# Performance work log

Measured on AMD Instinct MI355X. Metric: run time of the kernel, lower is better.

## Reference

```python
import jax, jax.numpy as jnp
import numpy as np

DIM = 384
H = 6
D = DIM // H
MLP = 4 * DIM
SCALE = D ** -0.5
LN_EPS = 1e-5


def _ln(x, w, b):
    m = jnp.mean(x, axis=-1, keepdims=True)
    v = jnp.mean((x - m) ** 2, axis=-1, keepdims=True)
    return (x - m) * jax.lax.rsqrt(v + LN_EPS) * w + b


def setup_inputs() -> dict:
    key = jax.random.key(0)
    ks = jax.random.split(key, 8)
    B, N = 8, 1024
    x = jax.random.normal(ks[0], (B, N, DIM), dtype=jnp.float32)
    # torch nn.Linear weights are [out, in]
    qkv_w = jax.random.normal(ks[1], (3 * DIM, DIM), dtype=jnp.float32) * (DIM ** -0.5)
    proj_w = jax.random.normal(ks[2], (DIM, DIM), dtype=jnp.float32) * (DIM ** -0.5)
    proj_b = jnp.zeros((DIM,), jnp.float32)
    # L2Q params, 'quadratic' init
    alpha = jnp.full((H, 1, 1), 0.125, jnp.float32)
    beta = jnp.full((H, 1, 1), 0.5, jnp.float32)
    gamma = jnp.zeros((H, 1, 1), jnp.float32)
    ln1_w = jnp.ones((DIM,), jnp.float32)
    ln1_b = jnp.zeros((DIM,), jnp.float32)
    ln2_w = jnp.ones((DIM,), jnp.float32)
    ln2_b = jnp.zeros((DIM,), jnp.float32)
    w1 = jax.random.normal(ks[3], (MLP, DIM), dtype=jnp.float32) * (DIM ** -0.5)
    b1 = jnp.zeros((MLP,), jnp.float32)
    w2 = jax.random.normal(ks[4], (DIM, MLP), dtype=jnp.float32) * (MLP ** -0.5)
    b2 = jnp.zeros((DIM,), jnp.float32)
    return {"x": x, "qkv_w": qkv_w, "proj_w": proj_w, "proj_b": proj_b,
            "alpha": alpha, "beta": beta, "gamma": gamma,
            "ln1_w": ln1_w, "ln1_b": ln1_b, "ln2_w": ln2_w, "ln2_b": ln2_b,
            "w1": w1, "b1": b1, "w2": w2, "b2": b2}


def reference(x, qkv_w, proj_w, proj_b, alpha, beta, gamma,
              ln1_w, ln1_b, ln2_w, ln2_b, w1, b1, w2, b2):
    B, N, C = x.shape
    # --- L2Q attention on LN(x) ---
    h = _ln(x, ln1_w, ln1_b)
    qkv = (h @ qkv_w.T).reshape(B, N, 3, H, D)
    q = qkv[:, :, 0].transpose(0, 2, 1, 3)  # [B,H,N,D]
    k = qkv[:, :, 1].transpose(0, 2, 1, 3)
    v = qkv[:, :, 2].transpose(0, 2, 1, 3)
    logits = jnp.einsum('bhnd,bhmd->bhnm', q, k) * SCALE
    attn = jax.nn.relu(alpha * logits ** 2 + beta * logits + gamma)
    attn = attn / (jnp.sum(attn, axis=-1, keepdims=True) + 1e-6)
    out = jnp.einsum('bhnm,bhmd->bhnd', attn, v)
    out = out.transpose(0, 2, 1, 3).reshape(B, N, C)
    x = x + out @ proj_w.T + proj_b
    # --- MLP on LN(x), exact GELU (torch default) ---
    h2 = _ln(x, ln2_w, ln2_b)
    m = jax.nn.gelu(h2 @ w1.T + b1, approximate=False)
    x = x + m @ w2.T + b2
    return x
```

## Files before the change

### kernel.cpp

```cpp
#include <hip/hip_runtime.h>
#include <hip/hip_bf16.h>
#include <math.h>

#define DIMC 384
#define NH 6
#define HD 64
#define MLPD 1536
#define BS 8
#define SEQ 1024
#define T_TOK (BS*SEQ)
#define TC ((size_t)T_TOK*DIMC)
#define QK_SCALE 0.125f

typedef __bf16 bf16;
typedef bf16 bf16x4 __attribute__((ext_vector_type(4)));
typedef bf16 bf16x8 __attribute__((ext_vector_type(8)));
typedef float floatx4 __attribute__((ext_vector_type(4)));

__device__ __forceinline__ void async_cp16(const void* gsrc, void* ldst) {
    __builtin_amdgcn_global_load_lds(
        (const __attribute__((address_space(1))) unsigned int*)gsrc,
        (__attribute__((address_space(3))) unsigned int*)ldst,
        16, 0, 0);
}

__global__ __launch_bounds__(256)
void cvt_all(const float* __restrict__ s0, const float* __restrict__ s1,
             const float* __restrict__ s2, const float* __restrict__ s3,
             bf16* __restrict__ dst) {
    int i = blockIdx.x * 256 + threadIdx.x;
    const int n0 = 110592, n1 = 36864, n2 = 147456;
    const float4* src; int j;
    if (i < n0)           { src = (const float4*)s0; j = i; }
    else if (i < n0+n1)   { src = (const float4*)s1; j = i - n0; }
    else if (i < n0+n1+n2){ src = (const float4*)s2; j = i - n0 - n1; }
    else                  { src = (const float4*)s3; j = i - n0 - n1 - n2; }
    float4 v = src[j];
    bf16x4 o; o[0] = (bf16)v.x; o[1] = (bf16)v.y; o[2] = (bf16)v.z; o[3] = (bf16)v.w;
    ((bf16x4*)dst)[i] = o;
}

__global__ __launch_bounds__(256)
void ln_kernel(const float* __restrict__ x, const float* __restrict__ w,
               const float* __restrict__ b, bf16* __restrict__ out) {
    int row = blockIdx.x * 4 + (threadIdx.x >> 6);
    int t = threadIdx.x & 63;
    const float* xr = x + (size_t)row * DIMC;
    float vals[6];
    float s = 0.f;
    #pragma unroll
    for (int i = 0; i < 6; i++) { vals[i] = xr[t + i*64]; s += vals[i]; }
    #pragma unroll
    for (int m = 32; m; m >>= 1) s += __shfl_xor(s, m);
    float mean = s * (1.0f / DIMC);
    float sq = 0.f;
    #pragma unroll
    for (int i = 0; i < 6; i++) { float d = vals[i] - mean; sq += d * d; }
    #pragma unroll
    for (int m = 32; m; m >>= 1) sq += __shfl_xor(sq, m);
    float rstd = rsqrtf(sq * (1.0f / DIMC) + 1e-5f);
    bf16* orow = out + (size_t)row * DIMC;
    #pragma unroll
    for (int i = 0; i < 6; i++) {
        int c = t + i*64;
        orow[c] = (bf16)((vals[i] - mean) * rstd * w[c] + b[c]);
    }
}

__global__ __launch_bounds__(256)
void ln2_fused(const float* __restrict__ x, const bf16* __restrict__ p0,
               const bf16* __restrict__ p1, const float* __restrict__ pb,
               const float* __restrict__ w, const float* __restrict__ b,
               float* __restrict__ x1, bf16* __restrict__ h) {
    int row = blockIdx.x * 4 + (threadIdx.x >> 6);
    int t = threadIdx.x & 63;
    size_t base = (size_t)row * DIMC;
    float vals[6];
    float s = 0.f;
    #pragma unroll
    for (int i = 0; i < 6; i++) {
        int c = t + i*64;
        float v = x[base + c] + (float)p0[base + c] + (float)p1[base + c] + pb[c];
        vals[i] = v; s += v;
    }
    #pragma unroll
    for (int m = 32; m; m >>= 1) s += __shfl_xor(s, m);
    float mean = s * (1.0f / DIMC);
    float sq = 0.f;
    #pragma unroll
    for (int i = 0; i < 6; i++) { float d = vals[i] - mean; sq += d * d; }
    #pragma unroll
    for (int m = 32; m; m >>= 1) sq += __shfl_xor(sq, m);
    float rstd = rsqrtf(sq * (1.0f / DIMC) + 1e-5f);
    #pragma unroll
    for (int i = 0; i < 6; i++) {
        int c = t + i*64;
        x1[base + c] = vals[i];
        h[base + c] = (bf16)((vals[i] - mean) * rstd * w[c] + b[c]);
    }
}

__global__ __launch_bounds__(256)
void reduce4(float* __restrict__ xo, const bf16* __restrict__ p0, const bf16* __restrict__ p1,
             const bf16* __restrict__ p2, const bf16* __restrict__ p3,
             const float* __restrict__ b2) {
    int i = blockIdx.x * 256 + threadIdx.x;
    float4 v = ((const float4*)xo)[i];
    int c = (i % 96) * 4;
    float4 bb = *(const float4*)(b2 + c);
    bf16x4 a0 = ((const bf16x4*)p0)[i], a1 = ((const bf16x4*)p1)[i];
    bf16x4 a2 = ((const bf16x4*)p2)[i], a3 = ((const bf16x4*)p3)[i];
    v.x += bb.x + (float)a0[0] + (float)a1[0] + (float)a2[0] + (float)a3[0];
    v.y += bb.y + (float)a0[1] + (float)a1[1] + (float)a2[1] + (float)a3[1];
    v.z += bb.z + (float)a0[2] + (float)a1[2] + (float)a2[2] + (float)a3[2];
    v.w += bb.w + (float)a0[3] + (float)a1[3] + (float)a2[3] + (float)a3[3];
    ((float4*)xo)[i] = v;
}

enum { EPI_NONE = 0, EPI_QKV = 1, EPI_GELU = 3 };

template<int EPI, int K, int KS, typename OutT>
__global__ __launch_bounds__(256)
void gemm_bt(const bf16* __restrict__ A, const bf16* __restrict__ W,
             const float* __restrict__ bias, OutT* out, int M, int N) {
    __shared__ __align__(16) bf16 Ash[128*32];
    __shared__ __align__(16) bf16 Bsh[128*32];
    constexpr int KB = K / KS;
    int tid = threadIdx.x;
    int lane = tid & 63, w = tid >> 6;
    int quad = lane >> 4, l16 = lane & 15;
    int rbase = blockIdx.y * 128 + (w >> 1) * 64;
    int cbase = blockIdx.x * 128 + (w & 1) * 64;
    int kbase = blockIdx.z * KB;
    int c1 = w * 64 + lane;
    int c2 = c1 + 256;
    const bf16* Ag1 = A + (size_t)(blockIdx.y*128 + (c1 >> 2)) * K + kbase + (c1 & 3) * 8;
    const bf16* Ag2 = A + (size_t)(blockIdx.y*128 + (c2 >> 2)) * K + kbase + (c2 & 3) * 8;
    const bf16* Wg1 = W + (size_t)(blockIdx.x*128 + (c1 >> 2)) * K + kbase + (c1 & 3) * 8;
    const bf16* Wg2 = W + (size_t)(blockIdx.x*128 + (c2 >> 2)) * K + kbase + (c2 & 3) * 8;
    bf16* As1 = Ash + c1 * 8;  bf16* As2 = Ash + c2 * 8;
    bf16* Bs1 = Bsh + c1 * 8;  bf16* Bs2 = Bsh + c2 * 8;

    int arow = (w >> 1) * 64;
    int brow = (w & 1) * 64;
    floatx4 acc[4][4] = {};
    #pragma unroll
    for (int kk = 0; kk < KB / 32; kk++) {
        __syncthreads();
        async_cp16(Ag1 + kk*32, As1);
        async_cp16(Ag2 + kk*32, As2);
        async_cp16(Wg1 + kk*32, Bs1);
        async_cp16(Wg2 + kk*32, Bs2);
        __syncthreads();
        bf16x8 a[4], bfr[4];
        #pragma unroll
        for (int tm = 0; tm < 4; tm++)
            a[tm] = *(const bf16x8*)&Ash[(arow + tm*16 + l16) * 32 + quad*8];
        #pragma unroll
        for (int tn = 0; tn < 4; tn++)
            bfr[tn] = *(const bf16x8*)&Bsh[(brow + tn*16 + l16) * 32 + quad*8];
        #pragma unroll
        for (int tm = 0; tm < 4; tm++)
            #pragma unroll
            for (int tn = 0; tn < 4; tn++)
                acc[tm][tn] = __builtin_amdgcn_mfma_f32_16x16x32_bf16(a[tm], bfr[tn], acc[tm][tn], 0, 0, 0);
    }

    #pragma unroll
    for (int tm = 0; tm < 4; tm++)
        #pragma unroll
        for (int tn = 0; tn < 4; tn++) {
            if constexpr (EPI == EPI_QKV) {
                int colb = cbase + tn*16 + l16;
                int which = colb / 384;
                int rowb = rbase + tm*16 + quad*4;
                int bb = rowb >> 10;
                if (which == 2) {
                    int rem = colb - 768;
                    int hh = rem >> 6, d = rem & 63;
                    int n = rowb & 1023;
                    bf16x4 pk;
                    #pragma unroll
                    for (int r = 0; r < 4; r++) pk[r] = (bf16)acc[tm][tn][r];
                    *(bf16x4*)((bf16*)out + 2*TC + (((size_t)(bb*NH + hh) * HD + d) << 10) + n) = pk;
                } else {
                    int rem = colb - which*384;
                    int hh = rem >> 6, d = rem & 63;
                    #pragma unroll
                    for (int r = 0; r < 4; r++) {
                        int n = (rowb & 1023) + r;
                        ((bf16*)out)[(size_t)which*TC + (((size_t)(bb*NH + hh) * SEQ + n) << 6) + d]
                            = (bf16)acc[tm][tn][r];
                    }
                }
            } else if constexpr (EPI == EPI_NONE) {
                OutT* ob = out + (size_t)blockIdx.z * M * N;
                #pragma unroll
                for (int r = 0; r < 4; r++) {
                    int row = rbase + tm*16 + quad*4 + r;
                    int col = cbase + tn*16 + l16;
                    ob[(size_t)row * N + col] = (OutT)acc[tm][tn][r];
                }
            } else {
                #pragma unroll
                for (int r = 0; r < 4; r++) {
                    int row = rbase + tm*16 + quad*4 + r;
                    int col = cbase + tn*16 + l16;
                    float v = acc[tm][tn][r] + bias[col];
                    v = 0.5f * v * (1.0f + erff(v * 0.70710678118f));
                    out[(size_t)row * N + col] = (OutT)v;
                }
            }
        }
}

__global__ __launch_bounds__(256)
void attn_kernel(const bf16* __restrict__ q, const bf16* __restrict__ k,
                 const bf16* __restrict__ vt, const float* __restrict__ alpha,
                 const float* __restrict__ beta, const float* __restrict__ gamma,
                 bf16* __restrict__ attn_out) {
    __shared__ __align__(16) char smem[52992];
    bf16  (*Psh)[72] = (bf16(*)[72])smem;
    float (*Ored)[68] = (float(*)[68])smem;
    float* rsred = (float*)(smem + 52224);

    int L = blockIdx.x;
    int xcd = L & 7, slot = L >> 3;
    int qt = slot & 15;
    int bh = xcd + ((slot >> 4) << 3);
    int bb = bh / NH, h = bh % NH;
    int q0 = qt * 64;
    int tid = threadIdx.x;
    int w = tid >> 6, lane = tid & 63, quad = lane >> 4, l16 = lane & 15;
    float av = alpha[h] * (QK_SCALE * QK_SCALE), bv = beta[h] * QK_SCALE, gv = gamma[h];
    const bf16* qb  = q  + (size_t)bh * SEQ * HD;
    const bf16* kb  = k  + (size_t)bh * SEQ * HD;
    const bf16* vtb = vt + (size_t)bh * HD * SEQ;

    bf16x8 qa[4][2];
    #pragma unroll
    for (int tm = 0; tm < 4; tm++)
        #pragma unroll
        for (int ks = 0; ks < 2; ks++)
            qa[tm][ks] = *(const bf16x8*)(qb + (size_t)(q0 + tm*16 + l16) * HD + ks*32 + quad*8);

    bf16x8 vone;
    #pragma unroll
    for (int j = 0; j < 8; j++) vone[j] = (bf16)1.0f;

    floatx4 o[4][4] = {};
    floatx4 rsacc[4] = {};
    int prow = w * 64;
    int rd_sw = ((l16 >> 2) & 3) << 3;

    for (int kt = w*4; kt < w*4 + 4; kt++) {
        int kb0 = kt * 64;
        bf16x8 kf[2][4];
        #pragma unroll
        for (int ks = 0; ks < 2; ks++)
            #pragma unroll
            for (int tn = 0; tn < 4; tn++)
                kf[ks][tn] = *(const bf16x8*)(kb + (size_t)(kb0 + tn*16 + l16) * HD + ks*32 + quad*8);
        #pragma unroll
        for (int tm = 0; tm < 4; tm++) {
            floatx4 s[4] = {};
            #pragma unroll
            for (int ks = 0; ks < 2; ks++)
                #pragma unroll
                for (int tn = 0; tn < 4; tn++)
                    s[tn] = __builtin_amdgcn_mfma_f32_16x16x32_bf16(qa[tm][ks], kf[ks][tn], s[tn], 0, 0, 0);
            #pragma unroll
            for (int tn = 0; tn < 4; tn++)
                #pragma unroll
                for (int r = 0; r < 4; r++) {
                    float xx = s[tn][r];
                    float p = fmaxf((av*xx + bv)*xx + gv, 0.f);
                    int row = tm*16 + quad*4 + r;
                    int col = (tn*16 + l16) ^ (quad << 3);
                    Psh[prow + row][col] = (bf16)p;
                }
        }
        #pragma unroll
        for (int ks = 0; ks < 2; ks++) {
            bf16x8 vf[4], pf[4];
            #pragma unroll
            for (int tn = 0; tn < 4; tn++)
                vf[tn] = *(const bf16x8*)(vtb + (size_t)(tn*16 + l16) * SEQ + kb0 + ks*32 + quad*8);
            #pragma unroll
            for (int tm = 0; tm < 4; tm++)
                pf[tm] = *(const bf16x8*)&Psh[prow + tm*16 + l16][(ks*32 + quad*8) ^ rd_sw];
            #pragma unroll
            for (int tm = 0; tm < 4; tm++)
                rsacc[tm] = __builtin_amdgcn_mfma_f32_16x16x32_bf16(pf[tm], vone, rsacc[tm], 0, 0, 0);
            #pragma unroll
            for (int tm = 0; tm < 4; tm++)
                #pragma unroll
                for (int tn = 0; tn < 4; tn++)
                    o[tm][tn] = __builtin_amdgcn_mfma_f32_16x16x32_bf16(pf[tm], vf[tn], o[tm][tn], 0, 0, 0);
        }
    }

    __syncthreads();
    if (w) {
        #pragma unroll
        for (int tm = 0; tm < 4; tm++) {
            #pragma unroll
            for (int tn = 0; tn < 4; tn++)
                #pragma unroll
                for (int r = 0; r < 4; r++)
                    Ored[(w-1)*64 + tm*16 + quad*4 + r][tn*16 + l16] = o[tm][tn][r];
            if (l16 == 0)
                #pragma unroll
                for (int r = 0; r < 4; r++)
                    rsred[(w-1)*64 + tm*16 + quad*4 + r] = rsacc[tm][r];
        }
    }
    __syncthreads();
    if (w == 0) {
        #pragma unroll
        for (int j = 0; j < 3; j++)
            #pragma unroll
            for (int tm = 0; tm < 4; tm++) {
                #pragma unroll
                for (int tn = 0; tn < 4; tn++)
                    #pragma unroll
                    for (int r = 0; r < 4; r++)
                        o[tm][tn][r] += Ored[j*64 + tm*16 + quad*4 + r][tn*16 + l16];
                #pragma unroll
                for (int r = 0; r < 4; r++)
                    rsacc[tm][r] += rsred[j*64 + tm*16 + quad*4 + r];
            }
        #pragma unroll
        for (int tm = 0; tm < 4; tm++)
            #pragma unroll
            for (int tn = 0; tn < 4; tn++)
                #pragma unroll
                for (int r = 0; r < 4; r++) {
                    int n = q0 + tm*16 + quad*4 + r;
                    attn_out[((size_t)(bb*SEQ + n)) * DIMC + h*HD + tn*16 + l16] =
                        (bf16)(o[tm][tn][r] / (rsacc[tm][r] + 1e-6f));
                }
    }
}

extern "C" void kernel_launch(void* const* d_in, const int* in_sizes, int n_in,
                              void* d_out, int out_size, void* d_ws, size_t ws_size,
                              hipStream_t stream) {
    const float* x      = (const float*)d_in[0];
    const float* qkv_w  = (const float*)d_in[1];
    const float* proj_w = (const float*)d_in[2];
    const float* proj_b = (const float*)d_in[3];
    const float* alpha  = (const float*)d_in[4];
    const float* beta   = (const float*)d_in[5];
    const float* gamma  = (const float*)d_in[6];
    const float* ln1_w  = (const float*)d_in[7];
    const float* ln1_b  = (const float*)d_in[8];
    const float* ln2_w  = (const float*)d_in[9];
    const float* ln2_b  = (const float*)d_in[10];
    const float* w1     = (const float*)d_in[11];
    const float* b1     = (const float*)d_in[12];
    const float* w2     = (const float*)d_in[13];
    const float* b2     = (const float*)d_in[14];
    float* out = (float*)d_out;

    char* base = (char*)d_ws;
    bf16* wq_bf = (bf16*)base;
    bf16* wp_bf = wq_bf + 442368;
    bf16* w1_bf = wq_bf + 589824;
    bf16* w2_bf = wq_bf + 1179648;
    bf16* h      = (bf16*)(base + 3538944);
    bf16* qkv    = (bf16*)(base + 9830400);
    bf16* attn_o = (bf16*)(base + 28704768);
    bf16* m      = qkv;
    bf16* Pp     = (bf16*)(base + 34996224);
    bf16* Pm     = (bf16*)(base + 34996224);

    cvt_all<<<1728, 256, 0, stream>>>(qkv_w, proj_w, w1, w2, wq_bf);
    ln_kernel<<<T_TOK/4, 256, 0, stream>>>(x, ln1_w, ln1_b, h);
    gemm_bt<EPI_QKV, 384, 1, bf16><<<dim3(9, 64, 1), 256, 0, stream>>>(
        h, wq_bf, nullptr, qkv, T_TOK, 1152);
    attn_kernel<<<768, 256, 0, stream>>>(
        qkv, qkv + TC, qkv + 2*TC, alpha, beta, gamma, attn_o);
    gemm_bt<EPI_NONE, 384, 2, bf16><<<dim3(3, 64, 2), 256, 0, stream>>>(
        attn_o, wp_bf, nullptr, Pp, T_TOK, DIMC);
    ln2_fused<<<T_TOK/4, 256, 0, stream>>>(x, Pp, Pp + TC, proj_b, ln2_w, ln2_b, out, h);
    gemm_bt<EPI_GELU, 384, 1, bf16><<<dim3(12, 64, 1), 256, 0, stream>>>(
        h, w1_bf, b1, m, T_TOK, MLPD);
    gemm_bt<EPI_NONE, 1536, 4, bf16><<<dim3(3, 64, 4), 256, 0, stream>>>(
        m, w2_bf, nullptr, Pm, T_TOK, DIMC);
    reduce4<<<TC/4/256, 256, 0, stream>>>(out, Pm, Pm + TC, Pm + 2*TC, Pm + 3*TC, b2);
}
```

Measured before the change: 244.0 us.

## Prefetch K tiles in attention and use tree reduction across waves

The attention kernel now fully unrolls the per-wave key-tile loop and issues the next tile's K loads ahead of the current tile's compute. V fragments are loaded before the score computation so their latency overlaps the QK MFMAs. The final cross-wave reduction becomes a two-level tree, with row sums stored in an extra column and the output rows split between two waves, which shrinks shared memory and spreads the epilogue. This adds register pressure from the kn and vf buffers and one more barrier.

```diff
diff --git a/kernel.cpp b/kernel.cpp
--- a/kernel.cpp
+++ b/kernel.cpp
@@ -219,10 +219,10 @@
                  const bf16* __restrict__ vt, const float* __restrict__ alpha,
                  const float* __restrict__ beta, const float* __restrict__ gamma,
                  bf16* __restrict__ attn_out) {
-    __shared__ __align__(16) char smem[52992];
+    __shared__ __align__(16) char smem[36864];
     bf16  (*Psh)[72] = (bf16(*)[72])smem;
-    float (*Ored)[68] = (float(*)[68])smem;
-    float* rsred = (float*)(smem + 52224);
+    float (*RedA)[68] = (float(*)[68])smem;
+    float (*RedB)[68] = RedA + 64;
 
     int L = blockIdx.x;
     int xcd = L & 7, slot = L >> 3;
@@ -252,15 +252,31 @@
     floatx4 rsacc[4] = {};
     int prow = w * 64;
     int rd_sw = ((l16 >> 2) & 3) << 3;
-
-    for (int kt = w*4; kt < w*4 + 4; kt++) {
-        int kb0 = kt * 64;
-        bf16x8 kf[2][4];
+    int kt_base = w * 4;
+
+    bf16x8 kf[2][4], kn[2][4], vf[2][4];
+    #pragma unroll
+    for (int ks = 0; ks < 2; ks++)
+        #pragma unroll
+        for (int tn = 0; tn < 4; tn++)
+            kf[ks][tn] = *(const bf16x8*)(kb + (size_t)(kt_base*64 + tn*16 + l16) * HD + ks*32 + quad*8);
+
+    #pragma unroll
+    for (int t = 0; t < 4; t++) {
+        int kb0 = (kt_base + t) * 64;
+        if (t < 3) {
+            int nb0 = kb0 + 64;
+            #pragma unroll
+            for (int ks = 0; ks < 2; ks++)
+                #pragma unroll
+                for (int tn = 0; tn < 4; tn++)
+                    kn[ks][tn] = *(const bf16x8*)(kb + (size_t)(nb0 + tn*16 + l16) * HD + ks*32 + quad*8);
+        }
         #pragma unroll
         for (int ks = 0; ks < 2; ks++)
             #pragma unroll
             for (int tn = 0; tn < 4; tn++)
-                kf[ks][tn] = *(const bf16x8*)(kb + (size_t)(kb0 + tn*16 + l16) * HD + ks*32 + quad*8);
+                vf[ks][tn] = *(const bf16x8*)(vtb + (size_t)(tn*16 + l16) * SEQ + kb0 + ks*32 + quad*8);
         #pragma unroll
         for (int tm = 0; tm < 4; tm++) {
             floatx4 s[4] = {};
@@ -282,10 +298,7 @@
         }
         #pragma unroll
         for (int ks = 0; ks < 2; ks++) {
-            bf16x8 vf[4], pf[4];
-            #pragma unroll
-            for (int tn = 0; tn < 4; tn++)
-                vf[tn] = *(const bf16x8*)(vtb + (size_t)(tn*16 + l16) * SEQ + kb0 + ks*32 + quad*8);
+            bf16x8 pf[4];
             #pragma unroll
             for (int tm = 0; tm < 4; tm++)
                 pf[tm] = *(const bf16x8*)&Psh[prow + tm*16 + l16][(ks*32 + quad*8) ^ rd_sw];
@@ -296,50 +309,109 @@
             for (int tm = 0; tm < 4; tm++)
                 #pragma unroll
                 for (int tn = 0; tn < 4; tn++)
-                    o[tm][tn] = __builtin_amdgcn_mfma_f32_16x16x32_bf16(pf[tm], vf[tn], o[tm][tn], 0, 0, 0);
+                    o[tm][tn] = __builtin_amdgcn_mfma_f32_16x16x32_bf16(pf[tm], vf[ks][tn], o[tm][tn], 0, 0, 0);
+        }
+        if (t < 3) {
+            #pragma unroll
+            for (int ks = 0; ks < 2; ks++)
+                #pragma unroll
+                for (int tn = 0; tn < 4; tn++)
+                    kf[ks][tn] = kn[ks][tn];
         }
     }
 
     __syncthreads();
-    if (w) {
+    if (w & 1) {
+        float (*R)[68] = (w == 1) ? RedA : RedB;
         #pragma unroll
         for (int tm = 0; tm < 4; tm++) {
             #pragma unroll
             for (int tn = 0; tn < 4; tn++)
                 #pragma unroll
                 for (int r = 0; r < 4; r++)
-                    Ored[(w-1)*64 + tm*16 + quad*4 + r][tn*16 + l16] = o[tm][tn][r];
+                    R[tm*16 + quad*4 + r][tn*16 + l16] = o[tm][tn][r];
             if (l16 == 0)
                 #pragma unroll
                 for (int r = 0; r < 4; r++)
-                    rsred[(w-1)*64 + tm*16 + quad*4 + r] = rsacc[tm][r];
+                    R[tm*16 + quad*4 + r][64] = rsacc[tm][r];
+        }
+    }
+    __syncthreads();
+    if (!(w & 1)) {
+        float (*R)[68] = (w == 0) ? RedA : RedB;
+        #pragma unroll
+        for (int tm = 0; tm < 4; tm++) {
+            #pragma unroll
+            for (int tn = 0; tn < 4; tn++)
+                #pragma unroll
+                for (int r = 0; r < 4; r++)
+                    o[tm][tn][r] += R[tm*16 + quad*4 + r][tn*16 + l16];
+            #pragma unroll
+            for (int r = 0; r < 4; r++)
+                rsacc[tm][r] += R[tm*16 + quad*4 + r][64];
+        }
+    }
+    __syncthreads();
+    if (w == 2) {
+        #pragma unroll
+        for (int tm = 0; tm < 2; tm++) {
+            #pragma unroll
+            for (int tn = 0; tn < 4; tn++)
+                #pragma unroll
+                for (int r = 0; r < 4; r++)
+                    RedA[tm*16 + quad*4 + r][tn*16 + l16] = o[tm][tn][r];
+            if (l16 == 0)
+                #pragma unroll
+                for (int r = 0; r < 4; r++)
+                    RedA[tm*16 + quad*4 + r][64] = rsacc[tm][r];
+        }
+    } else if (w == 0) {
+        #pragma unroll
+        for (int tm = 2; tm < 4; tm++) {
+            #pragma unroll
+            for (int tn = 0; tn < 4; tn++)
+                #pragma unroll
+                for (int r = 0; r < 4; r++)
+                    RedA[tm*16 + quad*4 + r][tn*16 + l16] = o[tm][tn][r];
+            if (l16 == 0)
+                #pragma unroll
+                for (int r = 0; r < 4; r++)
+                    RedA[tm*16 + quad*4 + r][64] = rsacc[tm][r];
         }
     }
     __syncthreads();
     if (w == 0) {
         #pragma unroll
-        for (int j = 0; j < 3; j++)
-            #pragma unroll
-            for (int tm = 0; tm < 4; tm++) {
-                #pragma unroll
-                for (int tn = 0; tn < 4; tn++)
-                    #pragma unroll
-                    for (int r = 0; r < 4; r++)
-                        o[tm][tn][r] += Ored[j*64 + tm*16 + quad*4 + r][tn*16 + l16];
-                #pragma unroll
-                for (int r = 0; r < 4; r++)
-                    rsacc[tm][r] += rsred[j*64 + tm*16 + quad*4 + r];
-            }
-        #pragma unroll
-        for (int tm = 0; tm < 4; tm++)
+        for (int tm = 0; tm < 2; tm++) {
+            #pragma unroll
+            for (int r = 0; r < 4; r++)
+                rsacc[tm][r] += RedA[tm*16 + quad*4 + r][64];
             #pragma unroll
             for (int tn = 0; tn < 4; tn++)
                 #pragma unroll
                 for (int r = 0; r < 4; r++) {
+                    float ov = o[tm][tn][r] + RedA[tm*16 + quad*4 + r][tn*16 + l16];
                     int n = q0 + tm*16 + quad*4 + r;
                     attn_out[((size_t)(bb*SEQ + n)) * DIMC + h*HD + tn*16 + l16] =
-                        (bf16)(o[tm][tn][r] / (rsacc[tm][r] + 1e-6f));
-                }
+                        (bf16)(ov / (rsacc[tm][r] + 1e-6f));
+                }
+        }
+    } else if (w == 2) {
+        #pragma unroll
+        for (int tm = 2; tm < 4; tm++) {
+            #pragma unroll
+            for (int r = 0; r < 4; r++)
+                rsacc[tm][r] += RedA[tm*16 + quad*4 + r][64];
+            #pragma unroll
+            for (int tn = 0; tn < 4; tn++)
+                #pragma unroll
+                for (int r = 0; r < 4; r++) {
+                    float ov = o[tm][tn][r] + RedA[tm*16 + quad*4 + r][tn*16 + l16];
+                    int n = q0 + tm*16 + quad*4 + r;
+                    attn_out[((size_t)(bb*SEQ + n)) * DIMC + h*HD + tn*16 + l16] =
+                        (bf16)(ov / (rsacc[tm][r] + 1e-6f));
+                }
+        }
     }
 }
 
```

Result: faster. 233.2 us (-4.4%).

## Restructure attention: split PV across head-dim per wave with shared P tiles

Applied to the files above, without the earlier changes.

Changes the attention kernel so that each wave computes scores for its own 64-key slice of a 256-key chunk into a shared P tile. All four waves then split the PV product along the head dimension, 16 output columns each, rather than each wave owning a quarter of the keys and reducing full 64x64 outputs through LDS at the end. Row sums are taken directly from the fp32 probabilities with shuffles instead of an extra MFMA against a ones vector. It also requests 2 blocks per SM through launch_bounds. The cost is two __syncthreads per chunk, and it drops the LDS swizzle, which may add bank conflicts.

```diff
diff --git a/kernel.cpp b/kernel.cpp
--- a/kernel.cpp
+++ b/kernel.cpp
@@ -214,15 +214,14 @@
         }
 }
 
-__global__ __launch_bounds__(256)
+__global__ __launch_bounds__(256, 2)
 void attn_kernel(const bf16* __restrict__ q, const bf16* __restrict__ k,
                  const bf16* __restrict__ vt, const float* __restrict__ alpha,
                  const float* __restrict__ beta, const float* __restrict__ gamma,
                  bf16* __restrict__ attn_out) {
-    __shared__ __align__(16) char smem[52992];
-    bf16  (*Psh)[72] = (bf16(*)[72])smem;
-    float (*Ored)[68] = (float(*)[68])smem;
-    float* rsred = (float*)(smem + 52224);
+    __shared__ __align__(16) bf16 Psh[64][264];
+    __shared__ float rsW[4][64];
+    __shared__ float rs_final[64];
 
     int L = blockIdx.x;
     int xcd = L & 7, slot = L >> 3;
@@ -237,110 +236,90 @@
     const bf16* kb  = k  + (size_t)bh * SEQ * HD;
     const bf16* vtb = vt + (size_t)bh * HD * SEQ;
 
-    bf16x8 qa[4][2];
-    #pragma unroll
-    for (int tm = 0; tm < 4; tm++)
-        #pragma unroll
-        for (int ks = 0; ks < 2; ks++)
-            qa[tm][ks] = *(const bf16x8*)(qb + (size_t)(q0 + tm*16 + l16) * HD + ks*32 + quad*8);
-
-    bf16x8 vone;
-    #pragma unroll
-    for (int j = 0; j < 8; j++) vone[j] = (bf16)1.0f;
-
-    floatx4 o[4][4] = {};
-    floatx4 rsacc[4] = {};
-    int prow = w * 64;
-    int rd_sw = ((l16 >> 2) & 3) << 3;
-
-    for (int kt = w*4; kt < w*4 + 4; kt++) {
-        int kb0 = kt * 64;
-        bf16x8 kf[2][4];
-        #pragma unroll
-        for (int ks = 0; ks < 2; ks++)
-            #pragma unroll
-            for (int tn = 0; tn < 4; tn++)
-                kf[ks][tn] = *(const bf16x8*)(kb + (size_t)(kb0 + tn*16 + l16) * HD + ks*32 + quad*8);
-        #pragma unroll
-        for (int tm = 0; tm < 4; tm++) {
+    floatx4 o[4] = {};
+    float rsp[4] = {0.f, 0.f, 0.f, 0.f};
+
+    bf16x8 kf[2][4];
+    #pragma unroll
+    for (int ks = 0; ks < 2; ks++)
+        #pragma unroll
+        for (int ksub = 0; ksub < 4; ksub++)
+            kf[ks][ksub] = *(const bf16x8*)(kb + (size_t)(w*64 + ksub*16 + l16) * HD + ks*32 + quad*8);
+
+    for (int c = 0; c < 4; c++) {
+        #pragma unroll
+        for (int qsub = 0; qsub < 4; qsub++) {
+            bf16x8 qa0 = *(const bf16x8*)(qb + (size_t)(q0 + qsub*16 + l16) * HD + quad*8);
+            bf16x8 qa1 = *(const bf16x8*)(qb + (size_t)(q0 + qsub*16 + l16) * HD + 32 + quad*8);
             floatx4 s[4] = {};
+            #pragma unroll
+            for (int ksub = 0; ksub < 4; ksub++)
+                s[ksub] = __builtin_amdgcn_mfma_f32_16x16x32_bf16(kf[0][ksub], qa0, s[ksub], 0, 0, 0);
+            #pragma unroll
+            for (int ksub = 0; ksub < 4; ksub++)
+                s[ksub] = __builtin_amdgcn_mfma_f32_16x16x32_bf16(kf[1][ksub], qa1, s[ksub], 0, 0, 0);
+            #pragma unroll
+            for (int ksub = 0; ksub < 4; ksub++) {
+                bf16x4 p4;
+                float rsum = 0.f;
+                #pragma unroll
+                for (int r = 0; r < 4; r++) {
+                    float xx = s[ksub][r];
+                    float p = fmaxf((av*xx + bv)*xx + gv, 0.f);
+                    p4[r] = (bf16)p;
+                    rsum += p;
+                }
+                rsp[qsub] += rsum;
+                *(bf16x4*)&Psh[qsub*16 + l16][w*64 + ksub*16 + quad*4] = p4;
+            }
+        }
+        __syncthreads();
+        if (c < 3) {
+            int kc = (c+1)*256 + w*64;
             #pragma unroll
             for (int ks = 0; ks < 2; ks++)
                 #pragma unroll
-                for (int tn = 0; tn < 4; tn++)
-                    s[tn] = __builtin_amdgcn_mfma_f32_16x16x32_bf16(qa[tm][ks], kf[ks][tn], s[tn], 0, 0, 0);
-            #pragma unroll
-            for (int tn = 0; tn < 4; tn++)
-                #pragma unroll
-                for (int r = 0; r < 4; r++) {
-                    float xx = s[tn][r];
-                    float p = fmaxf((av*xx + bv)*xx + gv, 0.f);
-                    int row = tm*16 + quad*4 + r;
-                    int col = (tn*16 + l16) ^ (quad << 3);
-                    Psh[prow + row][col] = (bf16)p;
-                }
-        }
-        #pragma unroll
-        for (int ks = 0; ks < 2; ks++) {
-            bf16x8 vf[4], pf[4];
-            #pragma unroll
-            for (int tn = 0; tn < 4; tn++)
-                vf[tn] = *(const bf16x8*)(vtb + (size_t)(tn*16 + l16) * SEQ + kb0 + ks*32 + quad*8);
-            #pragma unroll
-            for (int tm = 0; tm < 4; tm++)
-                pf[tm] = *(const bf16x8*)&Psh[prow + tm*16 + l16][(ks*32 + quad*8) ^ rd_sw];
-            #pragma unroll
-            for (int tm = 0; tm < 4; tm++)
-                rsacc[tm] = __builtin_amdgcn_mfma_f32_16x16x32_bf16(pf[tm], vone, rsacc[tm], 0, 0, 0);
-            #pragma unroll
-            for (int tm = 0; tm < 4; tm++)
-                #pragma unroll
-                for (int tn = 0; tn < 4; tn++)
-                    o[tm][tn] = __builtin_amdgcn_mfma_f32_16x16x32_bf16(pf[tm], vf[tn], o[tm][tn], 0, 0, 0);
-        }
-    }
-
+                for (int ksub = 0; ksub < 4; ksub++)
+                    kf[ks][ksub] = *(const bf16x8*)(kb + (size_t)(kc + ksub*16 + l16) * HD + ks*32 + quad*8);
+        }
+        const bf16* vrow = vtb + (size_t)(w*16 + l16) * SEQ + c*256;
+        #pragma unroll
+        for (int ksl = 0; ksl < 8; ksl++) {
+            bf16x8 vf = *(const bf16x8*)(vrow + ksl*32 + quad*8);
+            #pragma unroll
+            for (int qsub = 0; qsub < 4; qsub++) {
+                bf16x8 pf = *(const bf16x8*)&Psh[qsub*16 + l16][ksl*32 + quad*8];
+                o[qsub] = __builtin_amdgcn_mfma_f32_16x16x32_bf16(pf, vf, o[qsub], 0, 0, 0);
+            }
+        }
+        __syncthreads();
+    }
+
+    #pragma unroll
+    for (int qsub = 0; qsub < 4; qsub++) {
+        rsp[qsub] += __shfl_xor(rsp[qsub], 16);
+        rsp[qsub] += __shfl_xor(rsp[qsub], 32);
+    }
+    if (quad == 0) {
+        #pragma unroll
+        for (int qsub = 0; qsub < 4; qsub++)
+            rsW[w][qsub*16 + l16] = rsp[qsub];
+    }
     __syncthreads();
-    if (w) {
-        #pragma unroll
-        for (int tm = 0; tm < 4; tm++) {
-            #pragma unroll
-            for (int tn = 0; tn < 4; tn++)
-                #pragma unroll
-                for (int r = 0; r < 4; r++)
-                    Ored[(w-1)*64 + tm*16 + quad*4 + r][tn*16 + l16] = o[tm][tn][r];
-            if (l16 == 0)
-                #pragma unroll
-                for (int r = 0; r < 4; r++)
-                    rsred[(w-1)*64 + tm*16 + quad*4 + r] = rsacc[tm][r];
-        }
-    }
+    if (tid < 64)
+        rs_final[tid] = rsW[0][tid] + rsW[1][tid] + rsW[2][tid] + rsW[3][tid] + 1e-6f;
     __syncthreads();
-    if (w == 0) {
-        #pragma unroll
-        for (int j = 0; j < 3; j++)
-            #pragma unroll
-            for (int tm = 0; tm < 4; tm++) {
-                #pragma unroll
-                for (int tn = 0; tn < 4; tn++)
-                    #pragma unroll
-                    for (int r = 0; r < 4; r++)
-                        o[tm][tn][r] += Ored[j*64 + tm*16 + quad*4 + r][tn*16 + l16];
-                #pragma unroll
-                for (int r = 0; r < 4; r++)
-                    rsacc[tm][r] += rsred[j*64 + tm*16 + quad*4 + r];
-            }
-        #pragma unroll
-        for (int tm = 0; tm < 4; tm++)
-            #pragma unroll
-            for (int tn = 0; tn < 4; tn++)
-                #pragma unroll
-                for (int r = 0; r < 4; r++) {
-                    int n = q0 + tm*16 + quad*4 + r;
-                    attn_out[((size_t)(bb*SEQ + n)) * DIMC + h*HD + tn*16 + l16] =
-                        (bf16)(o[tm][tn][r] / (rsacc[tm][r] + 1e-6f));
-                }
-    }
+
+    #pragma unroll
+    for (int qsub = 0; qsub < 4; qsub++)
+        #pragma unroll
+        for (int r = 0; r < 4; r++) {
+            int ql = qsub*16 + quad*4 + r;
+            float rv = rs_final[ql];
+            int n = q0 + ql;
+            attn_out[((size_t)(bb*SEQ + n)) * DIMC + h*HD + w*16 + l16] =
+                (bf16)(o[qsub][r] / rv);
+        }
 }
 
 extern "C" void kernel_launch(void* const* d_in, const int* in_sizes, int n_in,
```

Result: faster. 228.5 us (-6.3%).
